# Kernel optimization log

Hardware: AMD Instinct MI355X
Metric: run time of the kernel (lower is better)

The kernel has to match this reference:

```python
import jax, jax.numpy as jnp
import numpy as np

N, E, F_IN, H, C = 100000, 1600000, 256, 256, 64
BN_EPS = 1e-5


def setup_inputs() -> dict:
    key = jax.random.key(0)
    ks = jax.random.split(key, 4)
    x = jax.random.normal(ks[0], (N, F_IN), dtype=jnp.float32)
    edge_index = jax.random.randint(ks[1], (2, E), 0, N, dtype=jnp.int32)
    W1 = jax.random.normal(ks[2], (F_IN, H), dtype=jnp.float32) / np.float32(np.sqrt(F_IN))
    b1 = jnp.zeros((H,), jnp.float32)
    gamma = jnp.ones((H,), jnp.float32)
    beta = jnp.zeros((H,), jnp.float32)
    running_mean = jnp.zeros((H,), jnp.float32)
    running_var = jnp.ones((H,), jnp.float32)
    W2 = jax.random.normal(ks[3], (H, C), dtype=jnp.float32) / np.float32(np.sqrt(H))
    b2 = jnp.zeros((C,), jnp.float32)
    return {"x": x, "edge_index": edge_index, "W1": W1, "b1": b1,
            "gamma": gamma, "beta": beta, "running_mean": running_mean,
            "running_var": running_var, "W2": W2, "b2": b2}


def gcn_conv(x, W, b, src, dst, n):
    """GCNConv with added self-loops and symmetric deg^-1/2 normalization."""
    h = x @ W  # [n, out]
    ones = jnp.ones((src.shape[0],), h.dtype)
    deg = jax.ops.segment_sum(ones, dst, num_segments=n) + 1.0  # +1 for self-loop
    dinv = jax.lax.rsqrt(deg)  # deg^{-1/2}
    coef = dinv[src] * dinv[dst]  # per-edge norm
    agg = jax.ops.segment_sum(h[src] * coef[:, None], dst, num_segments=n)
    # self-loop term: deg_i^{-1} * h_i
    return agg + h * (dinv * dinv)[:, None] + b


def reference(x, edge_index, W1, b1, gamma, beta, running_mean, running_var, W2, b2):
    src, dst = edge_index[0], edge_index[1]
    n = x.shape[0]
    h = gcn_conv(x, W1, b1, src, dst, n)
    # BatchNorm1d (eval mode, running stats) + ReLU; dropout is identity at inference
    h = (h - running_mean) * (gamma * jax.lax.rsqrt(running_var + BN_EPS)) + beta
    h = jax.nn.relu(h)
    return gcn_conv(h, W2, b2, src, dst, n)
```

## Files before the change

kernel.cpp:

```cpp
#include <hip/hip_runtime.h>

#define NNODES 100000
#define NEDGES 1600000
#define FIN 256
#define HDIM 256
#define CDIM 64
#define BN_EPS 1e-5f

#define EPB 4096
#define NBLK ((NEDGES + EPB - 1) / EPB)
#define NSEGS ((NNODES + 255) / 256)
#define SEGCAP 4608

typedef __attribute__((ext_vector_type(8))) short short8;
typedef __attribute__((ext_vector_type(8))) unsigned short ushort8_t;
typedef __attribute__((ext_vector_type(4))) float f32x4;

static __device__ __forceinline__ unsigned short f2bf(float f) {
  unsigned u = __float_as_uint(f);
  u += 0x7FFF + ((u >> 16) & 1);
  return (unsigned short)(u >> 16);
}
static __device__ __forceinline__ float bf2f(unsigned short h) {
  return __uint_as_float(((unsigned)h) << 16);
}


__global__ __launch_bounds__(256) void p1hist_k(const int* __restrict__ dst,
                                                unsigned* __restrict__ rank,
                                                int* __restrict__ bh) {
  __shared__ int lh[NSEGS];
  int b = blockIdx.x, t = threadIdx.x;
  for (int j = t; j < NSEGS; j += 256) lh[j] = 0;
  __syncthreads();
  int base = b * EPB;
  #pragma unroll
  for (int it = 0; it < EPB / 256; ++it) {
    int i = base + it * 256 + t;
    if (i < NEDGES) {
      int d = dst[i];
      int seg = d >> 8;
      int r = atomicAdd(&lh[seg], 1);
      rank[i] = ((unsigned)seg << 21) | ((unsigned)(d & 255) << 13) | (unsigned)r;
    }
  }
  __syncthreads();
  for (int j = t; j < NSEGS; j += 256) bh[j * NBLK + b] = lh[j];
}

__global__ __launch_bounds__(512) void p1scan_k(const int* __restrict__ bh,
                                                int* __restrict__ rowpref,
                                                int* __restrict__ segtot) {
  __shared__ int sm[512];
  int s = blockIdx.x, t = threadIdx.x;
  int v = (t < NBLK) ? bh[s * NBLK + t] : 0;
  sm[t] = v;
  __syncthreads();
  for (int off = 1; off < 512; off <<= 1) {
    int x = (t >= off) ? sm[t - off] : 0;
    __syncthreads();
    sm[t] += x;
    __syncthreads();
  }
  if (t < NBLK) rowpref[s * NBLK + t] = sm[t] - v;
  if (t == NBLK - 1) segtot[s] = sm[t];
}

__global__ __launch_bounds__(512) void segscan_k(const int* __restrict__ segtot,
                                                 int* __restrict__ segbase) {
  __shared__ int sm[512];
  int t = threadIdx.x;
  int v = (t < NSEGS) ? segtot[t] : 0;
  sm[t] = v;
  __syncthreads();
  for (int off = 1; off < 512; off <<= 1) {
    int x = (t >= off) ? sm[t - off] : 0;
    __syncthreads();
    sm[t] += x;
    __syncthreads();
  }
  if (t < NSEGS) segbase[t] = sm[t] - v;
  if (t == 0) segbase[NSEGS] = NEDGES;
}

__global__ __launch_bounds__(512) void p1scat_k(const int* __restrict__ src,
                                                const unsigned* __restrict__ rank,
                                                const int* __restrict__ rowpref,
                                                const int* __restrict__ segbase,
                                                unsigned* __restrict__ esort) {
  __shared__ int lh[512];
  __shared__ int sc[512];
  __shared__ int O[NSEGS];
  __shared__ unsigned sorted[EPB];
  __shared__ unsigned short segslot[EPB];
  int b = blockIdx.x, t = threadIdx.x;
  int base = b * EPB;
  lh[t] = 0;
  __syncthreads();
  unsigned wv[EPB / 512];
  #pragma unroll
  for (int it = 0; it < EPB / 512; ++it) {
    int i = base + it * 512 + t;
    wv[it] = 0xFFFFFFFFu;
    if (i < NEDGES) {
      wv[it] = rank[i];
      atomicAdd(&lh[wv[it] >> 21], 1);
    }
  }
  __syncthreads();
  int v = lh[t];
  sc[t] = v;
  __syncthreads();
  for (int off = 1; off < 512; off <<= 1) {
    int x = (t >= off) ? sc[t - off] : 0;
    __syncthreads();
    sc[t] += x;
    __syncthreads();
  }
  int excl = sc[t] - v;
  __syncthreads();
  lh[t] = excl;
  if (t < NSEGS) O[t] = segbase[t] + rowpref[t * NBLK + b] - excl;
  __syncthreads();
  #pragma unroll
  for (int it = 0; it < EPB / 512; ++it) {
    int i = base + it * 512 + t;
    if (i < NEDGES) {
      unsigned w = wv[it];
      int seg = w >> 21;
      int r = w & 8191;
      int d8 = (w >> 13) & 255;
      int slot = lh[seg] + r;
      sorted[slot] = ((unsigned)src[i] << 8) | (unsigned)d8;
      segslot[slot] = (unsigned short)seg;
    }
  }
  __syncthreads();
  int nE = NEDGES - base;
  if (nE > EPB) nE = EPB;
  for (int j = t; j < nE; j += 512) esort[O[segslot[j]] + j] = sorted[j];
}

__global__ __launch_bounds__(256) void p2_k(const unsigned* __restrict__ esort,
                                            const int* __restrict__ segtot,
                                            const int* __restrict__ segbase,
                                            int* __restrict__ s_sorted,
                                            int* __restrict__ ptr,
                                            float* __restrict__ dinv) {
  __shared__ unsigned ebuf[SEGCAP];
  __shared__ unsigned short lrank[SEGCAP];
  __shared__ int outbuf[SEGCAP];
  __shared__ int lcnt[256];
  __shared__ int sm[256];
  __shared__ int nstart[256];
  int s = blockIdx.x, t = threadIdx.x;
  int base = segbase[s];
  int cntE = segtot[s];
  if (cntE > SEGCAP) cntE = SEGCAP;
  for (int j = t; j < cntE; j += 256) ebuf[j] = esort[base + j];
  lcnt[t] = 0;
  __syncthreads();
  for (int j = t; j < cntE; j += 256) {
    int d8 = ebuf[j] & 255;
    lrank[j] = (unsigned short)atomicAdd(&lcnt[d8], 1);
  }
  __syncthreads();
  int v = lcnt[t];
  sm[t] = v;
  __syncthreads();
  for (int off = 1; off < 256; off <<= 1) {
    int x = (t >= off) ? sm[t - off] : 0;
    __syncthreads();
    sm[t] += x;
    __syncthreads();
  }
  nstart[t] = sm[t] - v;
  int node = s * 256 + t;
  if (node < NNODES) {
    ptr[node] = base + sm[t] - v;
    dinv[node] = rsqrtf((float)v + 1.0f);
  }
  __syncthreads();
  for (int j = t; j < cntE; j += 256) {
    unsigned w = ebuf[j];
    outbuf[nstart[w & 255] + lrank[j]] = (int)(w >> 8);
  }
  __syncthreads();
  for (int j = t; j < cntE; j += 256) s_sorted[base + j] = outbuf[j];
  if (s == 0 && t == 0) ptr[NNODES] = NEDGES;
}


__global__ void xbf_k(const float* __restrict__ x, unsigned short* __restrict__ xbf, int n4) {
  int i = blockIdx.x * blockDim.x + threadIdx.x;
  int stride = gridDim.x * blockDim.x;
  for (; i < n4; i += stride) {
    float4 v = reinterpret_cast<const float4*>(x)[i];
    reinterpret_cast<ushort4*>(xbf)[i] =
        make_ushort4(f2bf(v.x), f2bf(v.y), f2bf(v.z), f2bf(v.w));
  }
}

__global__ void split_wt_k(const float* __restrict__ W, unsigned short* __restrict__ hi,
                           unsigned short* __restrict__ lo, int K, int N) {
  int n = blockIdx.x;
  for (int k = threadIdx.x; k < K; k += blockDim.x) {
    float v = W[(size_t)k * N + n];
    unsigned short h = f2bf(v);
    hi[(size_t)n * K + k] = h;
    lo[(size_t)n * K + k] = f2bf(v - bf2f(h));
  }
}

__global__ void bn_prep_k(const float* __restrict__ b1, const float* __restrict__ gamma,
                          const float* __restrict__ beta, const float* __restrict__ rm,
                          const float* __restrict__ rv, float* __restrict__ bn_s,
                          float* __restrict__ bn_t) {
  int f = threadIdx.x;
  float s = gamma[f] * rsqrtf(rv[f] + BN_EPS);
  bn_s[f] = s;
  bn_t[f] = (b1[f] - rm[f]) * s + beta[f];
}


__global__ __launch_bounds__(256) void agg_x_k(
    const int* __restrict__ ptr, const int* __restrict__ ss,
    const float* __restrict__ dinv, const unsigned short* __restrict__ xbf,
    unsigned short* __restrict__ xhHi, int n) {
  int w = threadIdx.x >> 6;
  int lane = threadIdx.x & 63;
  int i = blockIdx.x * 4 + w;
  if (i >= n) return;
  int sub = lane >> 5;
  int f8 = (lane & 31) * 8;
  int beg = ptr[i], end = ptr[i + 1];
  float di = dinv[i];
  float a[8] = {};
  int e = beg;
  for (; e + 8 <= end; e += 8) {
    int s0 = ss[e + sub], s1 = ss[e + 2 + sub], s2 = ss[e + 4 + sub], s3 = ss[e + 6 + sub];
    float c0 = dinv[s0], c1 = dinv[s1], c2 = dinv[s2], c3 = dinv[s3];
    ushort8_t v0 = *reinterpret_cast<const ushort8_t*>(xbf + (size_t)s0 * FIN + f8);
    ushort8_t v1 = *reinterpret_cast<const ushort8_t*>(xbf + (size_t)s1 * FIN + f8);
    ushort8_t v2 = *reinterpret_cast<const ushort8_t*>(xbf + (size_t)s2 * FIN + f8);
    ushort8_t v3 = *reinterpret_cast<const ushort8_t*>(xbf + (size_t)s3 * FIN + f8);
    #pragma unroll
    for (int k = 0; k < 8; ++k)
      a[k] += c0 * bf2f(v0[k]) + c1 * bf2f(v1[k]) + c2 * bf2f(v2[k]) + c3 * bf2f(v3[k]);
  }
  for (; e < end; e += 2) {
    int idx = e + sub;
    if (idx < end) {
      int s = ss[idx];
      float c = dinv[s];
      ushort8_t v = *reinterpret_cast<const ushort8_t*>(xbf + (size_t)s * FIN + f8);
      #pragma unroll
      for (int k = 0; k < 8; ++k) a[k] += c * bf2f(v[k]);
    }
  }
  #pragma unroll
  for (int k = 0; k < 8; ++k) a[k] += __shfl_xor(a[k], 32);
  if (sub == 0) {
    ushort8_t vs = *reinterpret_cast<const ushort8_t*>(xbf + (size_t)i * FIN + f8);
    float di2 = di * di;
    ushort8_t o;
    #pragma unroll
    for (int k = 0; k < 8; ++k) o[k] = f2bf(a[k] * di + bf2f(vs[k]) * di2);
    *reinterpret_cast<ushort8_t*>(xhHi + (size_t)i * FIN + f8) = o;
  }
}


template <int BN, int EPI, bool ALO>
__global__ __launch_bounds__(256) void gemm_split_k(
    const unsigned short* __restrict__ Ahi, const unsigned short* __restrict__ Alo,
    const unsigned short* __restrict__ Bhi, const unsigned short* __restrict__ Blo,
    float* __restrict__ C, unsigned short* __restrict__ O1,
    unsigned short* __restrict__ O2, const float* __restrict__ bn_s,
    const float* __restrict__ bn_t, int M, int N, int K) {
  constexpr int WC = BN / 32;
  constexpr int ASZ = (ALO ? 2 : 1) * 128 * 64;
  __shared__ unsigned short smem[ASZ + 2 * BN * 64];
  unsigned short* aHi = smem;
  unsigned short* aLo = smem + 128 * 64;
  unsigned short* bHi = smem + ASZ;
  unsigned short* bLo = bHi + BN * 64;

  const int tid = threadIdx.x;
  const int w = tid >> 6;
  const int lane = tid & 63;
  const int wr = w >> 1, wc = w & 1;
  const int row0 = blockIdx.x * 128;
  const int col0 = blockIdx.y * BN;

  f32x4 acc[4][WC];
  #pragma unroll
  for (int mi = 0; mi < 4; ++mi)
    #pragma unroll
    for (int ni = 0; ni < WC; ++ni) {
      f32x4 z = {0.f, 0.f, 0.f, 0.f};
      acc[mi][ni] = z;
    }

  auto stage = [&](const unsigned short* G, unsigned short* Ld, int rows, int gr0,
                   int maxRow, int k0) {
    for (int i = 0; i < rows / 32; ++i) {
      int chunk = i * 256 + tid;
      int r = chunk >> 3;
      int c = chunk & 7;
      int cs = c ^ (r & 7);
      int gr = gr0 + r;
      if (gr > maxRow) gr = maxRow;
      const unsigned short* gp = G + (size_t)gr * K + k0 + cs * 8;
      unsigned short* lp = Ld + (i * 256 + w * 64) * 8;
      __builtin_amdgcn_global_load_lds((const __attribute__((address_space(1))) void*)gp,
                                       (__attribute__((address_space(3))) void*)lp, 16, 0, 0);
    }
  };

  for (int k0 = 0; k0 < K; k0 += 64) {
    stage(Ahi, aHi, 128, row0, M - 1, k0);
    if constexpr (ALO) stage(Alo, aLo, 128, row0, M - 1, k0);
    stage(Bhi, bHi, BN, col0, N - 1, k0);
    stage(Blo, bLo, BN, col0, N - 1, k0);
    __syncthreads();
    #pragma unroll
    for (int kk = 0; kk < 2; ++kk) {
      short8 ah[4], al[4], bh[WC], bl[WC];
      #pragma unroll
      for (int mi = 0; mi < 4; ++mi) {
        int lr = wr * 64 + mi * 16 + (lane & 15);
        int slot = (kk * 4 + (lane >> 4)) ^ (lr & 7);
        int eo = lr * 64 + slot * 8;
        ah[mi] = *reinterpret_cast<const short8*>(aHi + eo);
        if constexpr (ALO) al[mi] = *reinterpret_cast<const short8*>(aLo + eo);
      }
      #pragma unroll
      for (int ni = 0; ni < WC; ++ni) {
        int lr = wc * (BN / 2) + ni * 16 + (lane & 15);
        int slot = (kk * 4 + (lane >> 4)) ^ (lr & 7);
        int eo = lr * 64 + slot * 8;
        bh[ni] = *reinterpret_cast<const short8*>(bHi + eo);
        bl[ni] = *reinterpret_cast<const short8*>(bLo + eo);
      }
      #pragma unroll
      for (int mi = 0; mi < 4; ++mi)
        #pragma unroll
        for (int ni = 0; ni < WC; ++ni) {
          acc[mi][ni] = __builtin_amdgcn_mfma_f32_16x16x32_bf16(ah[mi], bh[ni], acc[mi][ni], 0, 0, 0);
          acc[mi][ni] = __builtin_amdgcn_mfma_f32_16x16x32_bf16(ah[mi], bl[ni], acc[mi][ni], 0, 0, 0);
          if constexpr (ALO)
            acc[mi][ni] = __builtin_amdgcn_mfma_f32_16x16x32_bf16(al[mi], bh[ni], acc[mi][ni], 0, 0, 0);
        }
    }
    __syncthreads();
  }

  #pragma unroll
  for (int ni = 0; ni < WC; ++ni) {
    int cc = col0 + wc * (BN / 2) + ni * 16 + (lane & 15);
    float sc = 0.f, tc = 0.f;
    if (EPI == 1) { sc = bn_s[cc]; tc = bn_t[cc]; }
    #pragma unroll
    for (int mi = 0; mi < 4; ++mi) {
      int rbase = row0 + wr * 64 + mi * 16 + (lane >> 4) * 4;
      #pragma unroll
      for (int r = 0; r < 4; ++r) {
        int rr = rbase + r;
        if (rr < M) {
          float v = acc[mi][ni][r];
          if (EPI == 1) {
            v = fmaxf(v * sc + tc, 0.f);
            unsigned short hv = f2bf(v);
            O1[(size_t)rr * N + cc] = hv;
            O2[(size_t)rr * N + cc] = f2bf(v - bf2f(hv));
          } else {
            C[(size_t)rr * N + cc] = v;
            O1[(size_t)rr * N + cc] = f2bf(v);
          }
        }
      }
    }
  }
}


__global__ __launch_bounds__(256) void agg2_k(
    const int* __restrict__ ptr, const int* __restrict__ ss,
    const float* __restrict__ dinv, const float* __restrict__ h2,
    const unsigned short* __restrict__ h2bf, const float* __restrict__ b2,
    float* __restrict__ out, int n) {
  int w = threadIdx.x >> 6;
  int lane = threadIdx.x & 63;
  int i = blockIdx.x * 4 + w;
  if (i >= n) return;
  int sub = lane >> 4;
  int f4 = (lane & 15) * 4;
  int beg = ptr[i], end = ptr[i + 1];
  float di = dinv[i];
  float a[4] = {};
  int e = beg;
  for (; e + 16 <= end; e += 16) {
    int s0 = ss[e + sub], s1 = ss[e + 4 + sub], s2 = ss[e + 8 + sub], s3 = ss[e + 12 + sub];
    float c0 = dinv[s0], c1 = dinv[s1], c2 = dinv[s2], c3 = dinv[s3];
    ushort4 v0 = *reinterpret_cast<const ushort4*>(h2bf + (size_t)s0 * CDIM + f4);
    ushort4 v1 = *reinterpret_cast<const ushort4*>(h2bf + (size_t)s1 * CDIM + f4);
    ushort4 v2 = *reinterpret_cast<const ushort4*>(h2bf + (size_t)s2 * CDIM + f4);
    ushort4 v3 = *reinterpret_cast<const ushort4*>(h2bf + (size_t)s3 * CDIM + f4);
    a[0] += c0 * bf2f(v0.x) + c1 * bf2f(v1.x) + c2 * bf2f(v2.x) + c3 * bf2f(v3.x);
    a[1] += c0 * bf2f(v0.y) + c1 * bf2f(v1.y) + c2 * bf2f(v2.y) + c3 * bf2f(v3.y);
    a[2] += c0 * bf2f(v0.z) + c1 * bf2f(v1.z) + c2 * bf2f(v2.z) + c3 * bf2f(v3.z);
    a[3] += c0 * bf2f(v0.w) + c1 * bf2f(v1.w) + c2 * bf2f(v2.w) + c3 * bf2f(v3.w);
  }
  for (; e < end; e += 4) {
    int idx = e + sub;
    if (idx < end) {
      int s = ss[idx];
      float c = dinv[s];
      ushort4 v = *reinterpret_cast<const ushort4*>(h2bf + (size_t)s * CDIM + f4);
      a[0] += c * bf2f(v.x); a[1] += c * bf2f(v.y);
      a[2] += c * bf2f(v.z); a[3] += c * bf2f(v.w);
    }
  }
  #pragma unroll
  for (int k = 0; k < 4; ++k) {
    a[k] += __shfl_xor(a[k], 16);
    a[k] += __shfl_xor(a[k], 32);
  }
  if (sub == 0) {
    float4 self = *reinterpret_cast<const float4*>(h2 + (size_t)i * CDIM + f4);
    float4 vb2 = *reinterpret_cast<const float4*>(b2 + f4);
    float di2 = di * di;
    float4 o;
    o.x = a[0] * di + self.x * di2 + vb2.x;
    o.y = a[1] * di + self.y * di2 + vb2.y;
    o.z = a[2] * di + self.z * di2 + vb2.z;
    o.w = a[3] * di + self.w * di2 + vb2.w;
    *reinterpret_cast<float4*>(out + (size_t)i * CDIM + f4) = o;
  }
}

extern "C" void kernel_launch(void* const* d_in, const int* in_sizes, int n_in,
                              void* d_out, int out_size, void* d_ws, size_t ws_size,
                              hipStream_t stream) {
  const float* x     = (const float*)d_in[0];
  const int*   ei    = (const int*)d_in[1];
  const float* W1    = (const float*)d_in[2];
  const float* b1    = (const float*)d_in[3];
  const float* gamma = (const float*)d_in[4];
  const float* beta  = (const float*)d_in[5];
  const float* rm    = (const float*)d_in[6];
  const float* rv    = (const float*)d_in[7];
  const float* W2    = (const float*)d_in[8];
  const float* b2    = (const float*)d_in[9];
  float* out = (float*)d_out;

  const int* src = ei;
  const int* dst = ei + NEDGES;

  char* ws = (char*)d_ws;
  auto alloc = [&](size_t bytes) {
    void* p = ws;
    ws += (bytes + 255) & ~(size_t)255;
    return p;
  };
  unsigned* rank    = (unsigned*)alloc((size_t)NEDGES * 4);
  unsigned* esort   = (unsigned*)alloc((size_t)NEDGES * 4);
  int*   bh       = (int*)alloc((size_t)NSEGS * NBLK * 4);
  int*   rowpref  = (int*)alloc((size_t)NSEGS * NBLK * 4);
  int*   segtot   = (int*)alloc((size_t)NSEGS * 4);
  int*   segbase  = (int*)alloc(((size_t)NSEGS + 1) * 4);
  int*   ptr      = (int*)alloc(((size_t)NNODES + 1) * 4);
  float* dinv     = (float*)alloc((size_t)NNODES * 4);
  int*   s_sorted = (int*)alloc((size_t)NEDGES * 4);
  unsigned short* xbf    = (unsigned short*)alloc((size_t)NNODES * FIN * 2);
  unsigned short* xhHi   = (unsigned short*)alloc((size_t)NNODES * FIN * 2);
  unsigned short* houtLo = (unsigned short*)alloc((size_t)NNODES * HDIM * 2);
  unsigned short* h2bf   = (unsigned short*)alloc((size_t)NNODES * CDIM * 2);
  unsigned short* w1thi  = (unsigned short*)alloc((size_t)HDIM * FIN * 2);
  unsigned short* w1tlo  = (unsigned short*)alloc((size_t)HDIM * FIN * 2);
  unsigned short* w2thi  = (unsigned short*)alloc((size_t)CDIM * HDIM * 2);
  unsigned short* w2tlo  = (unsigned short*)alloc((size_t)CDIM * HDIM * 2);
  float* bn_s = (float*)alloc(HDIM * 4);
  float* bn_t = (float*)alloc(HDIM * 4);

  unsigned short* houtHi = xbf;
  float*          h2     = (float*)xhHi;

  p1hist_k<<<NBLK, 256, 0, stream>>>(dst, rank, bh);
  p1scan_k<<<NSEGS, 512, 0, stream>>>(bh, rowpref, segtot);
  segscan_k<<<1, 512, 0, stream>>>(segtot, segbase);
  p1scat_k<<<NBLK, 512, 0, stream>>>(src, rank, rowpref, segbase, esort);
  p2_k<<<NSEGS, 256, 0, stream>>>(esort, segtot, segbase, s_sorted, ptr, dinv);

  xbf_k<<<12800, 256, 0, stream>>>(x, xbf, NNODES * FIN / 4);
  bn_prep_k<<<1, HDIM, 0, stream>>>(b1, gamma, beta, rm, rv, bn_s, bn_t);
  split_wt_k<<<HDIM, 256, 0, stream>>>(W1, w1thi, w1tlo, FIN, HDIM);
  split_wt_k<<<CDIM, 256, 0, stream>>>(W2, w2thi, w2tlo, HDIM, CDIM);

  agg_x_k<<<(NNODES + 3) / 4, 256, 0, stream>>>(ptr, s_sorted, dinv, xbf, xhHi, NNODES);
  gemm_split_k<128, 1, false><<<dim3((NNODES + 127) / 128, HDIM / 128), 256, 0, stream>>>(
      xhHi, nullptr, w1thi, w1tlo, nullptr, houtHi, houtLo, bn_s, bn_t, NNODES, HDIM, FIN);

  gemm_split_k<64, 2, true><<<dim3((NNODES + 127) / 128, 1), 256, 0, stream>>>(
      houtHi, houtLo, w2thi, w2tlo, h2, h2bf, nullptr, nullptr, nullptr, NNODES, CDIM, HDIM);
  agg2_k<<<(NNODES + 3) / 4, 256, 0, stream>>>(ptr, s_sorted, dinv, h2, h2bf, b2, out, NNODES);
}
```

Measured before the change: 356.5 us.

## Fold prep kernels into CSR build launches and drop hidden-activation low split

The x-to-bf16 conversion now runs as extra blocks of the histogram kernel, and the weight hi/lo split plus BN-parameter prep run as extra blocks of the per-segment scan kernel. This removes four separate launches and lets the independent work overlap with the graph-sort phase. Separately, the first GEMM no longer writes a bf16 low-residual copy of the hidden activations, and the second GEMM reads only the high part. That cuts a 51 MB write and read but lowers the precision of layer-2 inputs to plain bf16.

```diff
diff --git a/kernel.cpp b/kernel.cpp
--- a/kernel.cpp
+++ b/kernel.cpp
@@ -11,6 +11,7 @@
 #define NBLK ((NEDGES + EPB - 1) / EPB)
 #define NSEGS ((NNODES + 255) / 256)
 #define SEGCAP 4608
+#define XBLK 1600
 
 typedef __attribute__((ext_vector_type(8))) short short8;
 typedef __attribute__((ext_vector_type(8))) unsigned short ushort8_t;
@@ -27,10 +28,23 @@
 
 
 __global__ __launch_bounds__(256) void p1hist_k(const int* __restrict__ dst,
+                                                const float* __restrict__ x,
                                                 unsigned* __restrict__ rank,
-                                                int* __restrict__ bh) {
+                                                int* __restrict__ bh,
+                                                unsigned short* __restrict__ xbf) {
   __shared__ int lh[NSEGS];
   int b = blockIdx.x, t = threadIdx.x;
+  if (b >= NBLK) {
+    const int n4 = NNODES * FIN / 4;
+    int i = (b - NBLK) * 256 + t;
+    const int stride = XBLK * 256;
+    for (; i < n4; i += stride) {
+      float4 v = reinterpret_cast<const float4*>(x)[i];
+      reinterpret_cast<ushort4*>(xbf)[i] =
+          make_ushort4(f2bf(v.x), f2bf(v.y), f2bf(v.z), f2bf(v.w));
+    }
+    return;
+  }
   for (int j = t; j < NSEGS; j += 256) lh[j] = 0;
   __syncthreads();
   int base = b * EPB;
@@ -48,11 +62,43 @@
   for (int j = t; j < NSEGS; j += 256) bh[j * NBLK + b] = lh[j];
 }
 
-__global__ __launch_bounds__(512) void p1scan_k(const int* __restrict__ bh,
-                                                int* __restrict__ rowpref,
-                                                int* __restrict__ segtot) {
+__global__ __launch_bounds__(512) void p1scan_k(
+    const int* __restrict__ bh, int* __restrict__ rowpref, int* __restrict__ segtot,
+    const float* __restrict__ W1, const float* __restrict__ W2,
+    const float* __restrict__ b1, const float* __restrict__ gamma,
+    const float* __restrict__ beta, const float* __restrict__ rm,
+    const float* __restrict__ rv,
+    unsigned short* __restrict__ w1thi, unsigned short* __restrict__ w1tlo,
+    unsigned short* __restrict__ w2thi, unsigned short* __restrict__ w2tlo,
+    float* __restrict__ bn_s, float* __restrict__ bn_t) {
   __shared__ int sm[512];
   int s = blockIdx.x, t = threadIdx.x;
+  if (s >= NSEGS) {
+    int j = s - NSEGS;
+    if (j < HDIM) {
+      if (t < FIN) {
+        float v = W1[(size_t)t * HDIM + j];
+        unsigned short h = f2bf(v);
+        w1thi[(size_t)j * FIN + t] = h;
+        w1tlo[(size_t)j * FIN + t] = f2bf(v - bf2f(h));
+      }
+    } else if (j < HDIM + CDIM) {
+      int n = j - HDIM;
+      if (t < HDIM) {
+        float v = W2[(size_t)t * CDIM + n];
+        unsigned short h = f2bf(v);
+        w2thi[(size_t)n * HDIM + t] = h;
+        w2tlo[(size_t)n * HDIM + t] = f2bf(v - bf2f(h));
+      }
+    } else {
+      if (t < HDIM) {
+        float sc = gamma[t] * rsqrtf(rv[t] + BN_EPS);
+        bn_s[t] = sc;
+        bn_t[t] = (b1[t] - rm[t]) * sc + beta[t];
+      }
+    }
+    return;
+  }
   int v = (t < NBLK) ? bh[s * NBLK + t] : 0;
   sm[t] = v;
   __syncthreads();
@@ -188,38 +234,6 @@
   __syncthreads();
   for (int j = t; j < cntE; j += 256) s_sorted[base + j] = outbuf[j];
   if (s == 0 && t == 0) ptr[NNODES] = NEDGES;
-}
-
-
-__global__ void xbf_k(const float* __restrict__ x, unsigned short* __restrict__ xbf, int n4) {
-  int i = blockIdx.x * blockDim.x + threadIdx.x;
-  int stride = gridDim.x * blockDim.x;
-  for (; i < n4; i += stride) {
-    float4 v = reinterpret_cast<const float4*>(x)[i];
-    reinterpret_cast<ushort4*>(xbf)[i] =
-        make_ushort4(f2bf(v.x), f2bf(v.y), f2bf(v.z), f2bf(v.w));
-  }
-}
-
-__global__ void split_wt_k(const float* __restrict__ W, unsigned short* __restrict__ hi,
-                           unsigned short* __restrict__ lo, int K, int N) {
-  int n = blockIdx.x;
-  for (int k = threadIdx.x; k < K; k += blockDim.x) {
-    float v = W[(size_t)k * N + n];
-    unsigned short h = f2bf(v);
-    hi[(size_t)n * K + k] = h;
-    lo[(size_t)n * K + k] = f2bf(v - bf2f(h));
-  }
-}
-
-__global__ void bn_prep_k(const float* __restrict__ b1, const float* __restrict__ gamma,
-                          const float* __restrict__ beta, const float* __restrict__ rm,
-                          const float* __restrict__ rv, float* __restrict__ bn_s,
-                          float* __restrict__ bn_t) {
-  int f = threadIdx.x;
-  float s = gamma[f] * rsqrtf(rv[f] + BN_EPS);
-  bn_s[f] = s;
-  bn_t[f] = (b1[f] - rm[f]) * s + beta[f];
 }
 
 
@@ -276,8 +290,8 @@
     const unsigned short* __restrict__ Ahi, const unsigned short* __restrict__ Alo,
     const unsigned short* __restrict__ Bhi, const unsigned short* __restrict__ Blo,
     float* __restrict__ C, unsigned short* __restrict__ O1,
-    unsigned short* __restrict__ O2, const float* __restrict__ bn_s,
-    const float* __restrict__ bn_t, int M, int N, int K) {
+    const float* __restrict__ bn_s, const float* __restrict__ bn_t,
+    int M, int N, int K) {
   constexpr int WC = BN / 32;
   constexpr int ASZ = (ALO ? 2 : 1) * 128 * 64;
   __shared__ unsigned short smem[ASZ + 2 * BN * 64];
@@ -371,9 +385,7 @@
           float v = acc[mi][ni][r];
           if (EPI == 1) {
             v = fmaxf(v * sc + tc, 0.f);
-            unsigned short hv = f2bf(v);
-            O1[(size_t)rr * N + cc] = hv;
-            O2[(size_t)rr * N + cc] = f2bf(v - bf2f(hv));
+            O1[(size_t)rr * N + cc] = f2bf(v);
           } else {
             C[(size_t)rr * N + cc] = v;
             O1[(size_t)rr * N + cc] = f2bf(v);
@@ -475,7 +487,6 @@
   int*   s_sorted = (int*)alloc((size_t)NEDGES * 4);
   unsigned short* xbf    = (unsigned short*)alloc((size_t)NNODES * FIN * 2);
   unsigned short* xhHi   = (unsigned short*)alloc((size_t)NNODES * FIN * 2);
-  unsigned short* houtLo = (unsigned short*)alloc((size_t)NNODES * HDIM * 2);
   unsigned short* h2bf   = (unsigned short*)alloc((size_t)NNODES * CDIM * 2);
   unsigned short* w1thi  = (unsigned short*)alloc((size_t)HDIM * FIN * 2);
   unsigned short* w1tlo  = (unsigned short*)alloc((size_t)HDIM * FIN * 2);
@@ -487,22 +498,19 @@
   unsigned short* houtHi = xbf;
   float*          h2     = (float*)xhHi;
 
-  p1hist_k<<<NBLK, 256, 0, stream>>>(dst, rank, bh);
-  p1scan_k<<<NSEGS, 512, 0, stream>>>(bh, rowpref, segtot);
+  p1hist_k<<<NBLK + XBLK, 256, 0, stream>>>(dst, x, rank, bh, xbf);
+  p1scan_k<<<NSEGS + HDIM + CDIM + 1, 512, 0, stream>>>(
+      bh, rowpref, segtot, W1, W2, b1, gamma, beta, rm, rv,
+      w1thi, w1tlo, w2thi, w2tlo, bn_s, bn_t);
   segscan_k<<<1, 512, 0, stream>>>(segtot, segbase);
   p1scat_k<<<NBLK, 512, 0, stream>>>(src, rank, rowpref, segbase, esort);
   p2_k<<<NSEGS, 256, 0, stream>>>(esort, segtot, segbase, s_sorted, ptr, dinv);
 
-  xbf_k<<<12800, 256, 0, stream>>>(x, xbf, NNODES * FIN / 4);
-  bn_prep_k<<<1, HDIM, 0, stream>>>(b1, gamma, beta, rm, rv, bn_s, bn_t);
-  split_wt_k<<<HDIM, 256, 0, stream>>>(W1, w1thi, w1tlo, FIN, HDIM);
-  split_wt_k<<<CDIM, 256, 0, stream>>>(W2, w2thi, w2tlo, HDIM, CDIM);
-
   agg_x_k<<<(NNODES + 3) / 4, 256, 0, stream>>>(ptr, s_sorted, dinv, xbf, xhHi, NNODES);
   gemm_split_k<128, 1, false><<<dim3((NNODES + 127) / 128, HDIM / 128), 256, 0, stream>>>(
-      xhHi, nullptr, w1thi, w1tlo, nullptr, houtHi, houtLo, bn_s, bn_t, NNODES, HDIM, FIN);
-
-  gemm_split_k<64, 2, true><<<dim3((NNODES + 127) / 128, 1), 256, 0, stream>>>(
-      houtHi, houtLo, w2thi, w2tlo, h2, h2bf, nullptr, nullptr, nullptr, NNODES, CDIM, HDIM);
+      xhHi, nullptr, w1thi, w1tlo, nullptr, houtHi, bn_s, bn_t, NNODES, HDIM, FIN);
+
+  gemm_split_k<64, 2, false><<<dim3((NNODES + 127) / 128, 1), 256, 0, stream>>>(
+      houtHi, nullptr, w2thi, w2tlo, h2, h2bf, nullptr, nullptr, NNODES, CDIM, HDIM);
   agg2_k<<<(NNODES + 3) / 4, 256, 0, stream>>>(ptr, s_sorted, dinv, h2, h2bf, b2, out, NNODES);
 }
```

Result: faster. 318.8 us (-10.6%).
